# Optimization experiments

Measured on AMD Instinct MI355X. Metric: run time of the kernel, lower is better.

## Reference

```python
import jax, jax.numpy as jnp
import numpy as np

NORM = 1.0  # normalization_factor


def _glorot(key, shape):
    fan_in, fan_out = shape
    lim = float(np.sqrt(6.0 / (fan_in + fan_out)))
    return jax.random.uniform(key, shape, jnp.float32, -lim, lim)


def setup_inputs() -> dict:
    key = jax.random.key(0)
    ks = jax.random.split(key, 12)
    B, N = 8, 2048
    latent, hidden, out_dim = 64, 128, 64
    inp = {
        "latent_features": jax.random.normal(ks[0], (B, N, latent), jnp.float32),
        "adjacency_matrix": jax.random.uniform(ks[1], (B, N, N), jnp.float32),
        "node_mask": jnp.ones((B, N, 1), jnp.float32),
        # 3 GCN layers: latent->hidden, hidden->hidden, hidden->hidden
        "W0": _glorot(ks[2], (latent, hidden)), "b0": jnp.zeros((hidden,), jnp.float32),
        "W1": _glorot(ks[3], (hidden, hidden)), "b1": jnp.zeros((hidden,), jnp.float32),
        "W2": _glorot(ks[4], (hidden, hidden)), "b2": jnp.zeros((hidden,), jnp.float32),
        # output projection hidden->out_dim
        "Wout": _glorot(ks[5], (hidden, out_dim)), "bout": jnp.zeros((out_dim,), jnp.float32),
    }
    return inp


def _gcn_layer(h, adj, W, b):
    # message transform (linear), gather+sum aggregate via dense adjacency, ReLU act
    msg = h @ W + b                      # [B,N,dout]
    agg = jnp.einsum('bij,bjd->bid', adj, msg) / NORM  # sum aggregation over neighbors
    return jax.nn.relu(agg)


def reference(latent_features, adjacency_matrix, node_mask,
              W0, b0, W1, b1, W2, b2, Wout, bout):
    h = _gcn_layer(latent_features, adjacency_matrix, W0, b0)
    h = _gcn_layer(h, adjacency_matrix, W1, b1)
    h = _gcn_layer(h, adjacency_matrix, W2, b2)
    # output projection + node mask
    return (h @ Wout + bout) * node_mask
```

## Files before the change

kernel.cpp:

```cpp
#include <hip/hip_runtime.h>
#include <hip/hip_bf16.h>


typedef __bf16 bf16;
typedef __bf16 bf16x4 __attribute__((ext_vector_type(4)));
typedef __bf16 bf16x8 __attribute__((ext_vector_type(8)));
typedef float  f32x16 __attribute__((ext_vector_type(16)));
typedef float  f32x4  __attribute__((ext_vector_type(4)));

static __device__ inline f32x16 mfma32(bf16x8 a, bf16x8 b, f32x16 c) {
    return __builtin_amdgcn_mfma_f32_32x32x16_bf16(a, b, c, 0, 0, 0);
}

#define NB   8
#define NN   2048
#define LAT  64
#define HID  128
#define ODIM 64

__global__ __launch_bounds__(256) void prep_t0_k(
    const float* __restrict__ lat, const float* __restrict__ W0,
    const float* __restrict__ b0,
    const float* __restrict__ W1, const float* __restrict__ W2,
    const float* __restrict__ Wout,
    bf16* __restrict__ msgT, bf16* __restrict__ WT1,
    bf16* __restrict__ WT2, bf16* __restrict__ WoutT)
{
    __shared__ __align__(16) bf16 WTs[HID * 72];
    int tid = threadIdx.x;
    int blk = blockIdx.x;

    if (blk >= 256) {
        int i = (blk - 256) * 256 + tid;
        if (i < HID * HID) { int fo = i >> 7, k = i & 127; WT1[i] = (bf16)W1[k * HID + fo]; return; }
        i -= HID * HID;
        if (i < HID * HID) { int fo = i >> 7, k = i & 127; WT2[i] = (bf16)W2[k * HID + fo]; return; }
        i -= HID * HID;
        if (i < ODIM * HID) { int o = i >> 7, k = i & 127; WoutT[i] = (bf16)Wout[k * ODIM + o]; return; }
        return;
    }

    for (int i = tid; i < LAT * HID; i += 256) {
        int k = i >> 7, fo = i & 127;
        WTs[fo * 72 + k] = (bf16)W0[i];
    }
    __syncthreads();

    int l = tid & 63, w = tid >> 6;
    int lm = l & 31, lh = l >> 5;
    int g0 = blk * 64;
    int b  = g0 >> 11, nb = g0 & 2047;

    const bf16*  Wrow = &WTs[(w * 32 + lm) * 72 + lh * 8];
    const float* r0   = lat + (size_t)(g0 + lm) * LAT + lh * 8;
    const float* r1   = r0 + (size_t)32 * LAT;

    f32x16 acc0 = {}, acc1 = {};
#pragma unroll
    for (int k0 = 0; k0 < LAT; k0 += 16) {
        bf16x8 a = *(const bf16x8*)(Wrow + k0);
        f32x4 x0 = *(const f32x4*)(r0 + k0), x1 = *(const f32x4*)(r0 + k0 + 4);
        f32x4 y0 = *(const f32x4*)(r1 + k0), y1 = *(const f32x4*)(r1 + k0 + 4);
        bf16x8 v0, v1;
        v0[0]=(bf16)x0[0]; v0[1]=(bf16)x0[1]; v0[2]=(bf16)x0[2]; v0[3]=(bf16)x0[3];
        v0[4]=(bf16)x1[0]; v0[5]=(bf16)x1[1]; v0[6]=(bf16)x1[2]; v0[7]=(bf16)x1[3];
        v1[0]=(bf16)y0[0]; v1[1]=(bf16)y0[1]; v1[2]=(bf16)y0[2]; v1[3]=(bf16)y0[3];
        v1[4]=(bf16)y1[0]; v1[5]=(bf16)y1[1]; v1[6]=(bf16)y1[2]; v1[7]=(bf16)y1[3];
        acc0 = mfma32(a, v0, acc0);
        acc1 = mfma32(a, v1, acc1);
    }

    bf16* outb = msgT + (size_t)b * (HID * NN) + nb;
#pragma unroll
    for (int r = 0; r < 16; ++r) {
        int fo = w * 32 + (r & 3) + 8 * (r >> 2) + 4 * lh;
        float bv = b0[fo];
        outb[(size_t)fo * NN + lm]      = (bf16)(acc0[r] + bv);
        outb[(size_t)fo * NN + 32 + lm] = (bf16)(acc1[r] + bv);
    }
}

template<int MODE, int ADJW>
__global__ __launch_bounds__(256) void agg_k(
    const float* __restrict__ adjf, const bf16* __restrict__ adjbi,
    bf16* __restrict__ adjbo,
    const bf16* __restrict__ msgT, const bf16* __restrict__ WTn,
    const float* __restrict__ biasn, bf16* __restrict__ msg_out,
    const float* __restrict__ mask, float* __restrict__ out)
{
    __shared__ __align__(16) bf16 As[2][32 * 72];
    __shared__ __align__(16) bf16 Bs[2][128 * 72];
    __shared__ __align__(16) bf16 Hs[32 * 136];
    int tid = threadIdx.x;
    int l = tid & 63, w = tid >> 6;
    int lm = l & 31, lh = l >> 5;
    int b  = blockIdx.x & 7;
    int m0 = (blockIdx.x >> 3) * 32;

    const bf16* msgb = msgT + (size_t)b * (HID * NN);
    int br = tid >> 3, bc = (tid & 7) * 8;
    const bf16* bsrc = msgb + (size_t)br * NN + bc;

    int ar = tid >> 4, ac = (tid & 15) * 4;
    const float* asrc = (ADJW == 0) ? adjf + (size_t)b * NN * NN + (size_t)(m0 + ar) * NN + ac : nullptr;
    bf16* adst = (ADJW == 0) ? adjbo + (size_t)b * NN * NN + (size_t)(m0 + ar) * NN + ac : nullptr;
    int ar8 = tid >> 3, ac8 = (tid & 7) * 8;
    const bf16* asrcb = (ADJW == 1) ? adjbi + (size_t)b * NN * NN + (size_t)(m0 + ar8) * NN + ac8 : nullptr;

    f32x4  fa0[2], fa1[2];
    bf16x8 ba[2];
    bf16x8 pb[2][4];

    auto loadTile = [&](int set, int k) {
        if (ADJW == 0) {
            fa0[set] = *(const f32x4*)(asrc + k);
            fa1[set] = *(const f32x4*)(asrc + (size_t)16 * NN + k);
        } else {
            ba[set] = *(const bf16x8*)(asrcb + k);
        }
        pb[set][0] = *(const bf16x8*)(bsrc + k);
        pb[set][1] = *(const bf16x8*)(bsrc + (size_t)32 * NN + k);
        pb[set][2] = *(const bf16x8*)(bsrc + (size_t)64 * NN + k);
        pb[set][3] = *(const bf16x8*)(bsrc + (size_t)96 * NN + k);
    };
    auto storeTile = [&](int set, int buf, int k) {
        if (ADJW == 0) {
            bf16x4 v0, v1;
            v0[0]=(bf16)fa0[set][0]; v0[1]=(bf16)fa0[set][1]; v0[2]=(bf16)fa0[set][2]; v0[3]=(bf16)fa0[set][3];
            v1[0]=(bf16)fa1[set][0]; v1[1]=(bf16)fa1[set][1]; v1[2]=(bf16)fa1[set][2]; v1[3]=(bf16)fa1[set][3];
            *(bf16x4*)&As[buf][ar * 72 + ac]        = v0;
            *(bf16x4*)&As[buf][(ar + 16) * 72 + ac] = v1;
            *(bf16x4*)(adst + k)                    = v0;
            *(bf16x4*)(adst + (size_t)16 * NN + k)  = v1;
        } else {
            *(bf16x8*)&As[buf][ar8 * 72 + ac8] = ba[set];
        }
        *(bf16x8*)&Bs[buf][br * 72 + bc]        = pb[set][0];
        *(bf16x8*)&Bs[buf][(br + 32) * 72 + bc] = pb[set][1];
        *(bf16x8*)&Bs[buf][(br + 64) * 72 + bc] = pb[set][2];
        *(bf16x8*)&Bs[buf][(br + 96) * 72 + bc] = pb[set][3];
    };

    f32x16 acc = {};
    auto mfmaTile = [&](int buf) {
        const bf16* Ac = &As[buf][lm * 72 + lh * 8];
        const bf16* Bc = &Bs[buf][(w * 32 + lm) * 72 + lh * 8];
#pragma unroll
        for (int s = 0; s < 4; ++s)
            acc = mfma32(*(const bf16x8*)(Ac + s * 16), *(const bf16x8*)(Bc + s * 16), acc);
    };

    loadTile(0, 0);
    loadTile(1, 64);
    storeTile(0, 0, 0);
    __syncthreads();

#pragma unroll 1
    for (int kt = 0; kt < 32; kt += 2) {
        if (kt + 2 < 32) loadTile(0, (kt + 2) * 64);
        mfmaTile(0);
        storeTile(1, 1, (kt + 1) * 64);
        __syncthreads();
        if (kt + 3 < 32) loadTile(1, (kt + 3) * 64);
        mfmaTile(1);
        if (kt + 2 < 32) storeTile(0, 0, (kt + 2) * 64);
        __syncthreads();
    }

#pragma unroll
    for (int r = 0; r < 16; ++r) {
        int row = (r & 3) + 8 * (r >> 2) + 4 * lh;
        float v = acc[r];
        Hs[row * 136 + w * 32 + lm] = (bf16)(v > 0.f ? v : 0.f);
    }
    __syncthreads();

    if (MODE == 0) {
        const bf16* Arow = WTn + (size_t)(w * 32 + lm) * HID + lh * 8;
        const bf16* Brow = &Hs[lm * 136 + lh * 8];
        f32x16 acc2 = {};
#pragma unroll
        for (int s = 0; s < 8; ++s)
            acc2 = mfma32(*(const bf16x8*)(Arow + s * 16), *(const bf16x8*)(Brow + s * 16), acc2);
        bf16* outb = msg_out + (size_t)b * (HID * NN) + m0;
#pragma unroll
        for (int r = 0; r < 16; ++r) {
            int fo = w * 32 + (r & 3) + 8 * (r >> 2) + 4 * lh;
            outb[(size_t)fo * NN + lm] = (bf16)(acc2[r] + biasn[fo]);
        }
    } else {
        if (w < 2) {
            int ob = w * 32;
            const bf16* Arow = &Hs[lm * 136 + lh * 8];
            const bf16* Brow = WTn + (size_t)(ob + lm) * HID + lh * 8;
            f32x16 acc2 = {};
#pragma unroll
            for (int s = 0; s < 8; ++s)
                acc2 = mfma32(*(const bf16x8*)(Arow + s * 16), *(const bf16x8*)(Brow + s * 16), acc2);
            float bv = biasn[ob + lm];
#pragma unroll
            for (int r = 0; r < 16; ++r) {
                int node = (r & 3) + 8 * (r >> 2) + 4 * lh;
                int g = b * NN + m0 + node;
                out[(size_t)g * ODIM + ob + lm] = (acc2[r] + bv) * mask[g];
            }
        }
    }
}

extern "C" void kernel_launch(void* const* d_in, const int* in_sizes, int n_in,
                              void* d_out, int out_size, void* d_ws, size_t ws_size,
                              hipStream_t stream)
{
    const float* lat  = (const float*)d_in[0];
    const float* adj  = (const float*)d_in[1];
    const float* mask = (const float*)d_in[2];
    const float* W0   = (const float*)d_in[3];
    const float* b0   = (const float*)d_in[4];
    const float* W1   = (const float*)d_in[5];
    const float* b1   = (const float*)d_in[6];
    const float* W2   = (const float*)d_in[7];
    const float* b2   = (const float*)d_in[8];
    const float* Wout = (const float*)d_in[9];
    const float* bout = (const float*)d_in[10];
    float* out = (float*)d_out;

    char* ws = (char*)d_ws;
    bf16* msgA  = (bf16*)(ws + 0);
    bf16* msgB  = (bf16*)(ws + 4194304);
    bf16* adjbf = (bf16*)(ws + 8388608);
    bf16* WT1   = (bf16*)(ws + 75497472);
    bf16* WT2   = (bf16*)(ws + 75530240);
    bf16* WoutT = (bf16*)(ws + 75563008);

    prep_t0_k<<<416, 256, 0, stream>>>(lat, W0, b0, W1, W2, Wout, msgA, WT1, WT2, WoutT);

    agg_k<0, 0><<<512, 256, 0, stream>>>(adj, nullptr, adjbf, msgA, WT1, b1, msgB, nullptr, nullptr);
    agg_k<0, 1><<<512, 256, 0, stream>>>(nullptr, adjbf, nullptr, msgB, WT2, b2, msgA, nullptr, nullptr);
    agg_k<1, 1><<<512, 256, 0, stream>>>(nullptr, adjbf, nullptr, msgA, WoutT, bout, nullptr, mask, out);
}
```

Before: 283.6 us.

## Load MFMA operands directly from global memory, bypassing LDS staging

The aggregation kernel's main loop no longer stages adjacency and message tiles through double-buffered shared memory with barriers. Each lane now loads its MFMA fragments straight from global memory into registers, converting fp32 adjacency to bf16 in registers, and a register double-buffer is used for prefetch. This removes LDS traffic and the per-step __syncthreads. In exchange, all four waves redundantly load the same adjacency rows, global access is less coalesced (each lane reads 16-byte chunks strided across rows), and register pressure rises.

```diff
diff --git a/kernel.cpp b/kernel.cpp
--- a/kernel.cpp
+++ b/kernel.cpp
@@ -88,8 +88,6 @@
     const float* __restrict__ biasn, bf16* __restrict__ msg_out,
     const float* __restrict__ mask, float* __restrict__ out)
 {
-    __shared__ __align__(16) bf16 As[2][32 * 72];
-    __shared__ __align__(16) bf16 Bs[2][128 * 72];
     __shared__ __align__(16) bf16 Hs[32 * 136];
     int tid = threadIdx.x;
     int l = tid & 63, w = tid >> 6;
@@ -97,74 +95,67 @@
     int b  = blockIdx.x & 7;
     int m0 = (blockIdx.x >> 3) * 32;
 
-    const bf16* msgb = msgT + (size_t)b * (HID * NN);
-    int br = tid >> 3, bc = (tid & 7) * 8;
-    const bf16* bsrc = msgb + (size_t)br * NN + bc;
-
-    int ar = tid >> 4, ac = (tid & 15) * 4;
-    const float* asrc = (ADJW == 0) ? adjf + (size_t)b * NN * NN + (size_t)(m0 + ar) * NN + ac : nullptr;
-    bf16* adst = (ADJW == 0) ? adjbo + (size_t)b * NN * NN + (size_t)(m0 + ar) * NN + ac : nullptr;
-    int ar8 = tid >> 3, ac8 = (tid & 7) * 8;
-    const bf16* asrcb = (ADJW == 1) ? adjbi + (size_t)b * NN * NN + (size_t)(m0 + ar8) * NN + ac8 : nullptr;
-
-    f32x4  fa0[2], fa1[2];
-    bf16x8 ba[2];
-    bf16x8 pb[2][4];
-
-    auto loadTile = [&](int set, int k) {
+    const bf16* bptr = msgT + (size_t)b * (HID * NN) + (size_t)(w * 32 + lm) * NN + lh * 8;
+    const float* aptrf = (ADJW == 0) ? adjf  + (size_t)b * NN * NN + (size_t)(m0 + lm) * NN + lh * 8 : nullptr;
+    const bf16*  aptrb = (ADJW == 1) ? adjbi + (size_t)b * NN * NN + (size_t)(m0 + lm) * NN + lh * 8 : nullptr;
+    bf16*        awb   = (ADJW == 0) ? adjbo + (size_t)b * NN * NN + (size_t)(m0 + lm) * NN + lh * 8 : nullptr;
+
+    f32x16 acc = {};
+    bf16x8 aA[4], aB[4], pA[4], pB[4];
+    f32x4  fA[8], fB[8];
+
+    auto ldA = [&](bf16x8* a, f32x4* f, int k) {
         if (ADJW == 0) {
-            fa0[set] = *(const f32x4*)(asrc + k);
-            fa1[set] = *(const f32x4*)(asrc + (size_t)16 * NN + k);
+#pragma unroll
+            for (int s = 0; s < 4; ++s) {
+                f[2*s]   = *(const f32x4*)(aptrf + k + s * 16);
+                f[2*s+1] = *(const f32x4*)(aptrf + k + s * 16 + 4);
+            }
         } else {
-            ba[set] = *(const bf16x8*)(asrcb + k);
-        }
-        pb[set][0] = *(const bf16x8*)(bsrc + k);
-        pb[set][1] = *(const bf16x8*)(bsrc + (size_t)32 * NN + k);
-        pb[set][2] = *(const bf16x8*)(bsrc + (size_t)64 * NN + k);
-        pb[set][3] = *(const bf16x8*)(bsrc + (size_t)96 * NN + k);
-    };
-    auto storeTile = [&](int set, int buf, int k) {
+#pragma unroll
+            for (int s = 0; s < 4; ++s) a[s] = *(const bf16x8*)(aptrb + k + s * 16);
+        }
+    };
+    auto ldB = [&](bf16x8* p, int k) {
+#pragma unroll
+        for (int s = 0; s < 4; ++s) p[s] = *(const bf16x8*)(bptr + k + s * 16);
+    };
+    auto cvtA = [&](bf16x8* a, const f32x4* f, int k) {
         if (ADJW == 0) {
-            bf16x4 v0, v1;
-            v0[0]=(bf16)fa0[set][0]; v0[1]=(bf16)fa0[set][1]; v0[2]=(bf16)fa0[set][2]; v0[3]=(bf16)fa0[set][3];
-            v1[0]=(bf16)fa1[set][0]; v1[1]=(bf16)fa1[set][1]; v1[2]=(bf16)fa1[set][2]; v1[3]=(bf16)fa1[set][3];
-            *(bf16x4*)&As[buf][ar * 72 + ac]        = v0;
-            *(bf16x4*)&As[buf][(ar + 16) * 72 + ac] = v1;
-            *(bf16x4*)(adst + k)                    = v0;
-            *(bf16x4*)(adst + (size_t)16 * NN + k)  = v1;
-        } else {
-            *(bf16x8*)&As[buf][ar8 * 72 + ac8] = ba[set];
-        }
-        *(bf16x8*)&Bs[buf][br * 72 + bc]        = pb[set][0];
-        *(bf16x8*)&Bs[buf][(br + 32) * 72 + bc] = pb[set][1];
-        *(bf16x8*)&Bs[buf][(br + 64) * 72 + bc] = pb[set][2];
-        *(bf16x8*)&Bs[buf][(br + 96) * 72 + bc] = pb[set][3];
-    };
-
-    f32x16 acc = {};
-    auto mfmaTile = [&](int buf) {
-        const bf16* Ac = &As[buf][lm * 72 + lh * 8];
-        const bf16* Bc = &Bs[buf][(w * 32 + lm) * 72 + lh * 8];
-#pragma unroll
-        for (int s = 0; s < 4; ++s)
-            acc = mfma32(*(const bf16x8*)(Ac + s * 16), *(const bf16x8*)(Bc + s * 16), acc);
-    };
-
-    loadTile(0, 0);
-    loadTile(1, 64);
-    storeTile(0, 0, 0);
-    __syncthreads();
+#pragma unroll
+            for (int s = 0; s < 4; ++s) {
+                bf16x8 v;
+                v[0]=(bf16)f[2*s][0];   v[1]=(bf16)f[2*s][1];   v[2]=(bf16)f[2*s][2];   v[3]=(bf16)f[2*s][3];
+                v[4]=(bf16)f[2*s+1][0]; v[5]=(bf16)f[2*s+1][1]; v[6]=(bf16)f[2*s+1][2]; v[7]=(bf16)f[2*s+1][3];
+                a[s] = v;
+                if (w == 0) *(bf16x8*)(awb + k + s * 16) = v;
+            }
+        }
+    };
+    auto mfma4 = [&](const bf16x8* a, const bf16x8* p) {
+#pragma unroll
+        for (int s = 0; s < 4; ++s) acc = mfma32(a[s], p[s], acc);
+    };
+
+    ldA(aA, fA, 0);   ldB(pA, 0);
+    ldA(aB, fB, 64);  ldB(pB, 64);
 
 #pragma unroll 1
     for (int kt = 0; kt < 32; kt += 2) {
-        if (kt + 2 < 32) loadTile(0, (kt + 2) * 64);
-        mfmaTile(0);
-        storeTile(1, 1, (kt + 1) * 64);
-        __syncthreads();
-        if (kt + 3 < 32) loadTile(1, (kt + 3) * 64);
-        mfmaTile(1);
-        if (kt + 2 < 32) storeTile(0, 0, (kt + 2) * 64);
-        __syncthreads();
+        cvtA(aA, fA, kt * 64);
+        if (ADJW == 0 && kt + 2 < 32) ldA(aA, fA, (kt + 2) * 64);
+        mfma4(aA, pA);
+        if (kt + 2 < 32) {
+            if (ADJW != 0) ldA(aA, fA, (kt + 2) * 64);
+            ldB(pA, (kt + 2) * 64);
+        }
+        cvtA(aB, fB, (kt + 1) * 64);
+        if (ADJW == 0 && kt + 3 < 32) ldA(aB, fB, (kt + 3) * 64);
+        mfma4(aB, pB);
+        if (kt + 3 < 32) {
+            if (ADJW != 0) ldA(aB, fB, (kt + 3) * 64);
+            ldB(pB, (kt + 3) * 64);
+        }
     }
 
 #pragma unroll
```

Result: slower. 416.5 us (+46.8%).
